# Kernel optimization log

Hardware: AMD Instinct MI355X
Metric: run time of the kernel (lower is better)

Reference implementation:

```python
import jax, jax.numpy as jnp
import numpy as np

N_NODES = 50000


def gcn_layer(x, W, b, src, dst, num_nodes):
    """PyG-style GCNConv: add self-loops, symmetric normalization, linear, scatter-add, bias."""
    # linear transform first (PyG applies lin before propagate)
    h = x @ W  # [N, out]
    # add self loops
    loop = jnp.arange(num_nodes, dtype=src.dtype)
    s = jnp.concatenate([src, loop])  # [E+N]
    d = jnp.concatenate([dst, loop])  # [E+N]
    # degree of target nodes (with self loops)
    deg = jax.ops.segment_sum(jnp.ones_like(d, dtype=h.dtype), d, num_segments=num_nodes)
    dis = jnp.where(deg > 0, jax.lax.rsqrt(deg), 0.0)  # deg^{-1/2}
    norm = dis[s] * dis[d]  # [E+N]
    msg = h[s] * norm[:, None]  # gather + scale: [E+N, out]
    out = jax.ops.segment_sum(msg, d, num_segments=num_nodes)  # scatter-add
    return out + b


def setup_inputs() -> dict:
    key = jax.random.key(0)
    ks = jax.random.split(key, 8)
    n, e = N_NODES, 800000
    in_c, hid_c, out_c = 64, 128, 64
    x = jax.random.normal(ks[0], (n, in_c), dtype=jnp.float32)
    edge_index = jax.random.randint(ks[1], (2, e), 0, n, dtype=jnp.int64)
    def glorot(k, fan_in, fan_out):
        lim = np.sqrt(6.0 / (fan_in + fan_out)).astype(np.float32)
        return jax.random.uniform(k, (fan_in, fan_out), jnp.float32, -lim, lim)
    return {
        "x": x,
        "edge_index": edge_index,
        "W1": glorot(ks[2], in_c, hid_c), "b1": jnp.zeros((hid_c,), jnp.float32),
        "W2": glorot(ks[3], hid_c, hid_c), "b2": jnp.zeros((hid_c,), jnp.float32),
        "W3": glorot(ks[4], hid_c, out_c), "b3": jnp.zeros((out_c,), jnp.float32),
    }


def reference(x, edge_index, W1, b1, W2, b2, W3, b3):
    src, dst = edge_index[0], edge_index[1]
    n = x.shape[0]
    h = gcn_layer(x, W1, b1, src, dst, n)
    h = jax.nn.relu(h)
    h = gcn_layer(h, W2, b2, src, dst, n)
    h = jax.nn.relu(h)
    return gcn_layer(h, W3, b3, src, dst, n)
```

## Files before the change

### kernel.cpp

```cpp
#include <hip/hip_runtime.h>
#include <hip/hip_fp16.h>


typedef _Float16 h8 __attribute__((ext_vector_type(8)));
typedef float f32x4 __attribute__((ext_vector_type(4)));

struct alignas(8) Half4 { __half2 lo, hi; };

__device__ inline float4 h4_to_f4(Half4 h) {
    float2 a = __half22float2(h.lo), b = __half22float2(h.hi);
    return make_float4(a.x, a.y, b.x, b.y);
}
__device__ inline Half4 f4_to_h4(float4 v) {
    Half4 h; h.lo = __floats2half2_rn(v.x, v.y); h.hi = __floats2half2_rn(v.z, v.w); return h;
}

#define MAXNB 512


__global__ __launch_bounds__(256) void bucket_count(const int* __restrict__ dst,
                                                    int* __restrict__ bcnt, int e, int nb) {
    __shared__ int h[MAXNB];
    int tid = threadIdx.x;
    for (int i = tid; i < nb; i += 256) h[i] = 0;
    __syncthreads();
    for (int i = blockIdx.x * 256 + tid; i < e; i += gridDim.x * 256)
        atomicAdd(&h[dst[i] >> 7], 1);
    __syncthreads();
    for (int i = tid; i < nb; i += 256) {
        int c = h[i];
        if (c) atomicAdd(&bcnt[i], c);
    }
}


__global__ void scan_buckets(const int* __restrict__ bcnt, int* __restrict__ bbase,
                             int* __restrict__ bcursor, int nb) {
    int lane = threadIdx.x;
    int running = 0;
    for (int base = 0; base < nb; base += 64) {
        int idx = base + lane;
        int v = (idx < nb) ? bcnt[idx] : 0;
        int x = v;
        #pragma unroll
        for (int d = 1; d < 64; d <<= 1) {
            int t = __shfl_up(x, d, 64);
            if (lane >= d) x += t;
        }
        if (idx < nb) { bbase[idx] = running + x - v; bcursor[idx] = running + x - v; }
        running += __shfl(x, 63, 64);
    }
    if (lane == 0) bbase[nb] = running;
}


#define R3_CHUNK 4096

__global__ __launch_bounds__(256) void bin_edges(const int* __restrict__ src,
                                                 const int* __restrict__ dst,
                                                 int* __restrict__ bcursor,
                                                 int2* __restrict__ binned, int e, int nb) {
    __shared__ int h[MAXNB];
    __shared__ int gp[MAXNB];
    int tid = threadIdx.x;
    for (int i = tid; i < nb; i += 256) h[i] = 0;
    __syncthreads();
    int lo = blockIdx.x * R3_CHUNK, hi = min(lo + R3_CHUNK, e);
    for (int i = lo + tid; i < hi; i += 256) atomicAdd(&h[dst[i] >> 7], 1);
    __syncthreads();
    for (int b = tid; b < nb; b += 256) {
        int c = h[b];
        if (c) gp[b] = atomicAdd(&bcursor[b], c);
        h[b] = 0;
    }
    __syncthreads();
    for (int i = lo + tid; i < hi; i += 256) {
        int d = dst[i];
        int b = d >> 7;
        int p = atomicAdd(&h[b], 1);
        binned[gp[b] + p] = make_int2(src[i], d);
    }
}


__global__ __launch_bounds__(128) void finalize_csr(const int2* __restrict__ binned,
                                                    const int* __restrict__ bbase,
                                                    int* __restrict__ offsets,
                                                    int* __restrict__ srcs,
                                                    float* __restrict__ dis,
                                                    int n, int nb) {
    int b = blockIdx.x;
    int tid = threadIdx.x;
    int nb0 = b << 7;
    int segLo = bbase[b], segHi = bbase[b + 1];

    __shared__ int cnt[128];
    __shared__ int cur[128];
    __shared__ int wtot;
    cnt[tid] = 0;
    __syncthreads();
    for (int i = segLo + tid; i < segHi; i += 128)
        atomicAdd(&cnt[binned[i].y & 127], 1);
    __syncthreads();

    int c = cnt[tid];
    int lane = tid & 63, w = tid >> 6;
    int x = c;
    #pragma unroll
    for (int d = 1; d < 64; d <<= 1) {
        int t = __shfl_up(x, d, 64);
        if (lane >= d) x += t;
    }
    if (w == 0 && lane == 63) wtot = x;
    __syncthreads();
    int excl = x - c + (w ? wtot : 0);

    int node = nb0 + tid;
    if (node < n) {
        offsets[node] = segLo + excl;
        dis[node] = rsqrtf((float)(c + 1));
    }
    if (b == nb - 1 && tid == 0) offsets[n] = segHi;
    cur[tid] = excl;
    __syncthreads();

    for (int i = segLo + tid; i < segHi; i += 128) {
        int2 v = binned[i];
        int ln = v.y & 127;
        int p = atomicAdd(&cur[ln], 1);
        srcs[segLo + p] = v.x;
    }
}


__global__ __launch_bounds__(256) void prep_x_kernel(const float* __restrict__ x,
                                                     const float* __restrict__ dis,
                                                     Half4* __restrict__ x16, int n) {
    int gid = blockIdx.x * 256 + threadIdx.x;
    int total = n * 16;
    if (gid >= total) return;
    int node = gid >> 4;
    float4 v = reinterpret_cast<const float4*>(x)[gid];
    float d = dis[node];
    x16[gid] = f4_to_h4(make_float4(v.x * d, v.y * d, v.z * d, v.w * d));
}


template<int C, bool RELU, bool BIAS, bool OUTH>
__global__ __launch_bounds__(256) void aggregate_h(const __half* __restrict__ g,
                                                   const int* __restrict__ srcs,
                                                   const int* __restrict__ offsets,
                                                   const float* __restrict__ dis,
                                                   const float* __restrict__ bias,
                                                   void* __restrict__ outv, int n) {
    int wid = threadIdx.x >> 6, lane = threadIdx.x & 63;
    int i = blockIdx.x * 4 + wid;
    if (i >= n) return;
    float di = dis[i];
    int e0 = offsets[i], e1 = offsets[i + 1];
    int e = e0;

    if constexpr (C == 128) {
        int half_ = lane >> 5, cl = lane & 31, c = cl * 4;
        const Half4* gc = reinterpret_cast<const Half4*>(g) + cl;
        float4 a0 = make_float4(0.f, 0.f, 0.f, 0.f), a1v = a0, a2 = a0, a3 = a0;

        if (half_ == 0) a0 = h4_to_f4(gc[(size_t)i * 32]);

        for (; e + 8 <= e1; e += 8) {
            int s0 = srcs[e + half_], s1 = srcs[e + 2 + half_];
            int s2 = srcs[e + 4 + half_], s3 = srcs[e + 6 + half_];
            float4 l0 = h4_to_f4(gc[(size_t)s0 * 32]);
            float4 l1 = h4_to_f4(gc[(size_t)s1 * 32]);
            float4 l2 = h4_to_f4(gc[(size_t)s2 * 32]);
            float4 l3 = h4_to_f4(gc[(size_t)s3 * 32]);
            a0.x += l0.x; a0.y += l0.y; a0.z += l0.z; a0.w += l0.w;
            a1v.x += l1.x; a1v.y += l1.y; a1v.z += l1.z; a1v.w += l1.w;
            a2.x += l2.x; a2.y += l2.y; a2.z += l2.z; a2.w += l2.w;
            a3.x += l3.x; a3.y += l3.y; a3.z += l3.z; a3.w += l3.w;
        }
        if (e + 4 <= e1) {
            int s0 = srcs[e + half_], s1 = srcs[e + 2 + half_];
            float4 l0 = h4_to_f4(gc[(size_t)s0 * 32]);
            float4 l1 = h4_to_f4(gc[(size_t)s1 * 32]);
            a0.x += l0.x; a0.y += l0.y; a0.z += l0.z; a0.w += l0.w;
            a1v.x += l1.x; a1v.y += l1.y; a1v.z += l1.z; a1v.w += l1.w;
            e += 4;
        }
        if (e + 2 <= e1) {
            int s0 = srcs[e + half_];
            float4 l0 = h4_to_f4(gc[(size_t)s0 * 32]);
            a2.x += l0.x; a2.y += l0.y; a2.z += l0.z; a2.w += l0.w;
            e += 2;
        }
        if (e < e1 && half_ == 0) {
            int s0 = srcs[e];
            float4 l0 = h4_to_f4(gc[(size_t)s0 * 32]);
            a3.x += l0.x; a3.y += l0.y; a3.z += l0.z; a3.w += l0.w;
        }

        float4 acc = make_float4((a0.x + a1v.x) + (a2.x + a3.x), (a0.y + a1v.y) + (a2.y + a3.y),
                                 (a0.z + a1v.z) + (a2.z + a3.z), (a0.w + a1v.w) + (a2.w + a3.w));
        acc.x += __shfl_xor(acc.x, 32, 64);
        acc.y += __shfl_xor(acc.y, 32, 64);
        acc.z += __shfl_xor(acc.z, 32, 64);
        acc.w += __shfl_xor(acc.w, 32, 64);

        if (half_ == 0) {
            float4 o = make_float4(di * acc.x, di * acc.y, di * acc.z, di * acc.w);
            if constexpr (BIAS) {
                float4 b = *reinterpret_cast<const float4*>(bias + c);
                o.x += b.x; o.y += b.y; o.z += b.z; o.w += b.w;
            }
            if constexpr (RELU) {
                o.x = fmaxf(o.x, 0.f); o.y = fmaxf(o.y, 0.f);
                o.z = fmaxf(o.z, 0.f); o.w = fmaxf(o.w, 0.f);
            }
            if constexpr (OUTH)
                *reinterpret_cast<Half4*>((__half*)outv + (size_t)i * C + c) = f4_to_h4(o);
            else
                *reinterpret_cast<float4*>((float*)outv + (size_t)i * C + c) = o;
        }
    } else {
        int grp = lane >> 4, cl = lane & 15, c = cl * 4;
        const Half4* gc = reinterpret_cast<const Half4*>(g) + cl;
        float4 a0 = make_float4(0.f, 0.f, 0.f, 0.f), a1v = a0;

        if (grp == 0) a0 = h4_to_f4(gc[(size_t)i * 16]);

        for (; e + 8 <= e1; e += 8) {
            int s0 = srcs[e + grp], s1 = srcs[e + 4 + grp];
            float4 l0 = h4_to_f4(gc[(size_t)s0 * 16]);
            float4 l1 = h4_to_f4(gc[(size_t)s1 * 16]);
            a0.x += l0.x; a0.y += l0.y; a0.z += l0.z; a0.w += l0.w;
            a1v.x += l1.x; a1v.y += l1.y; a1v.z += l1.z; a1v.w += l1.w;
        }
        if (e + 4 <= e1) {
            int s0 = srcs[e + grp];
            float4 l0 = h4_to_f4(gc[(size_t)s0 * 16]);
            a0.x += l0.x; a0.y += l0.y; a0.z += l0.z; a0.w += l0.w;
            e += 4;
        }
        int rem = e1 - e;
        if (grp < rem) {
            int s0 = srcs[e + grp];
            float4 l0 = h4_to_f4(gc[(size_t)s0 * 16]);
            a1v.x += l0.x; a1v.y += l0.y; a1v.z += l0.z; a1v.w += l0.w;
        }

        float4 acc = make_float4(a0.x + a1v.x, a0.y + a1v.y, a0.z + a1v.z, a0.w + a1v.w);
        #pragma unroll
        for (int d = 16; d <= 32; d <<= 1) {
            acc.x += __shfl_xor(acc.x, d, 64);
            acc.y += __shfl_xor(acc.y, d, 64);
            acc.z += __shfl_xor(acc.z, d, 64);
            acc.w += __shfl_xor(acc.w, d, 64);
        }

        if (grp == 0) {
            float4 o = make_float4(di * acc.x, di * acc.y, di * acc.z, di * acc.w);
            if constexpr (BIAS) {
                float4 b = *reinterpret_cast<const float4*>(bias + c);
                o.x += b.x; o.y += b.y; o.z += b.z; o.w += b.w;
            }
            if constexpr (RELU) {
                o.x = fmaxf(o.x, 0.f); o.y = fmaxf(o.y, 0.f);
                o.z = fmaxf(o.z, 0.f); o.w = fmaxf(o.w, 0.f);
            }
            if constexpr (OUTH)
                *reinterpret_cast<Half4*>((__half*)outv + (size_t)i * C + c) = f4_to_h4(o);
            else
                *reinterpret_cast<float4*>((float*)outv + (size_t)i * C + c) = o;
        }
    }
}


template<int CIN, int COUT>
__global__ __launch_bounds__(256) void pack_w(const float* __restrict__ W, h8* __restrict__ Wp) {
    constexpr int NKS = CIN / 32, NCT = COUT / 16;
    int idx = blockIdx.x * 256 + threadIdx.x;
    if (idx >= NKS * NCT * 64) return;
    int l = idx & 63;
    int ct = (idx >> 6) % NCT;
    int ks = (idx >> 6) / NCT;
    int col = ct * 16 + (l & 15);
    int kb = ks * 32 + ((l >> 4) << 2);
    h8 t;
    #pragma unroll
    for (int j = 0; j < 8; ++j) {
        int k = kb + (j & 3) + ((j >> 2) << 4);
        t[j] = (_Float16)W[k * COUT + col];
    }
    Wp[idx] = t;
}


template<int CIN, int COUT, int EPI>
__global__ __launch_bounds__(256) void mfma_gemm(const __half* __restrict__ A,
                                                 const h8* __restrict__ Wp,
                                                 const float* __restrict__ aux,
                                                 __half* __restrict__ out, int n) {
    constexpr int NKS = CIN / 32, NCT = COUT / 16;
    constexpr int FRAGS = NKS * NCT * 64;
    __shared__ h8 wlds[FRAGS];
    for (int idx = threadIdx.x; idx < FRAGS; idx += 256) wlds[idx] = Wp[idx];
    __syncthreads();

    int wid = threadIdx.x >> 6, lane = threadIdx.x & 63;
    int rowBase = blockIdx.x * 128 + wid * 32;
    int m = lane & 15;
    int kq = (lane >> 4) << 2;

    int row0 = min(rowBase + m, n - 1);
    int row1 = min(rowBase + 16 + m, n - 1);
    const __half* ar0 = A + (size_t)row0 * CIN;
    const __half* ar1 = A + (size_t)row1 * CIN;

    f32x4 acc[2][NCT];
    #pragma unroll
    for (int rt = 0; rt < 2; ++rt)
        #pragma unroll
        for (int ct = 0; ct < NCT; ++ct)
            acc[rt][ct] = f32x4{0.f, 0.f, 0.f, 0.f};

    #pragma unroll
    for (int ks = 0; ks < NKS; ++ks) {
        int kb = ks * 32 + kq;
        h8 a0, a1;
        *reinterpret_cast<short4*>(&a0) = *reinterpret_cast<const short4*>(ar0 + kb);
        *(reinterpret_cast<short4*>(&a0) + 1) = *reinterpret_cast<const short4*>(ar0 + kb + 16);
        *reinterpret_cast<short4*>(&a1) = *reinterpret_cast<const short4*>(ar1 + kb);
        *(reinterpret_cast<short4*>(&a1) + 1) = *reinterpret_cast<const short4*>(ar1 + kb + 16);
        #pragma unroll
        for (int ct = 0; ct < NCT; ++ct) {
            h8 b = wlds[(ks * NCT + ct) * 64 + lane];
            acc[0][ct] = __builtin_amdgcn_mfma_f32_16x16x32_f16(a0, b, acc[0][ct], 0, 0, 0);
            acc[1][ct] = __builtin_amdgcn_mfma_f32_16x16x32_f16(a1, b, acc[1][ct], 0, 0, 0);
        }
    }

    float bcol[NCT];
    if constexpr (EPI == 1) {
        #pragma unroll
        for (int ct = 0; ct < NCT; ++ct) bcol[ct] = aux[ct * 16 + m];
    }
    #pragma unroll
    for (int rt = 0; rt < 2; ++rt) {
        #pragma unroll
        for (int r = 0; r < 4; ++r) {
            int row = rowBase + rt * 16 + kq + r;
            if (row < n) {
                float d = 0.f;
                if constexpr (EPI == 0) d = aux[row];
                __half* orow = out + (size_t)row * COUT + m;
                #pragma unroll
                for (int ct = 0; ct < NCT; ++ct) {
                    float v = acc[rt][ct][r];
                    if constexpr (EPI == 0) v *= d;
                    else v = fmaxf(v + bcol[ct], 0.f);
                    orow[ct * 16] = __float2half(v);
                }
            }
        }
    }
}


extern "C" void kernel_launch(void* const* d_in, const int* in_sizes, int n_in,
                              void* d_out, int out_size, void* d_ws, size_t ws_size,
                              hipStream_t stream) {
    const float* x  = (const float*)d_in[0];
    const int*   ei = (const int*)d_in[1];
    const float* W1 = (const float*)d_in[2];
    const float* b1 = (const float*)d_in[3];
    const float* W2 = (const float*)d_in[4];
    const float* b2 = (const float*)d_in[5];
    const float* W3 = (const float*)d_in[6];
    const float* b3 = (const float*)d_in[7];

    const int n = in_sizes[0] / 64;
    const int e = in_sizes[1] / 2;
    const int* src = ei;
    const int* dst = ei + e;
    const int nb = (n + 127) >> 7;

    int*   ws_i = (int*)d_ws;
    float* ws_f = (float*)d_ws;
    size_t o = 0;
    int* bcnt    = ws_i + o; o += MAXNB;
    int* bbase   = ws_i + o; o += MAXNB + 2;
    int* bcursor = ws_i + o; o += MAXNB;
    int* offsets = ws_i + o; o += n + 8;
    int* srcs    = ws_i + o; o += e;
    float* dis   = ws_f + o; o += n;
    o = (o + 1) & ~(size_t)1;
    int2* binned = (int2*)(ws_i + o); o += (size_t)e * 2;
    o = (o + 3) & ~(size_t)3;
    h8* Wp1 = (h8*)(ws_i + o); o += 4096;
    h8* Wp2 = (h8*)(ws_i + o); o += 8192;
    h8* Wp3 = (h8*)(ws_i + o); o += 4096;
    float* R1 = ws_f + o; o += (size_t)n * 64;
    float* R2 = ws_f + o; o += (size_t)n * 64;

    Half4*  x16 = (Half4*)d_out;
    __half* g2  = (__half*)d_out;
    __half* a1h = (__half*)R1;
    __half* h1h = (__half*)R2;
    __half* h2h = (__half*)R1;
    __half* g3  = (__half*)R2;
    float*  out = (float*)d_out;

    const int B = 256;
    hipMemsetAsync(bcnt, 0, MAXNB * sizeof(int), stream);
    bucket_count<<<256, B, 0, stream>>>(dst, bcnt, e, nb);
    scan_buckets<<<1, 64, 0, stream>>>(bcnt, bbase, bcursor, nb);
    bin_edges<<<(e + R3_CHUNK - 1) / R3_CHUNK, B, 0, stream>>>(src, dst, bcursor, binned, e, nb);
    finalize_csr<<<nb, 128, 0, stream>>>(binned, bbase, offsets, srcs, dis, n, nb);
    prep_x_kernel<<<(n * 16 + B - 1) / B, B, 0, stream>>>(x, dis, x16, n);
    pack_w<64, 128><<<4, B, 0, stream>>>(W1, Wp1);
    pack_w<128, 128><<<8, B, 0, stream>>>(W2, Wp2);
    pack_w<128, 64><<<4, B, 0, stream>>>(W3, Wp3);

    dim3 agrid((n + 3) / 4);
    dim3 ggrid((n + 127) / 128);

    aggregate_h<64, false, false, true><<<agrid, 256, 0, stream>>>((const __half*)x16, srcs, offsets, dis, nullptr, a1h, n);
    mfma_gemm<64, 128, 1><<<ggrid, 256, 0, stream>>>(a1h, Wp1, b1, h1h, n);
    mfma_gemm<128, 128, 0><<<ggrid, 256, 0, stream>>>(h1h, Wp2, dis, g2, n);
    aggregate_h<128, true, true, true><<<agrid, 256, 0, stream>>>(g2, srcs, offsets, dis, b2, h2h, n);
    mfma_gemm<128, 64, 0><<<ggrid, 256, 0, stream>>>(h2h, Wp3, dis, g3, n);
    aggregate_h<64, false, true, false><<<agrid, 256, 0, stream>>>(g3, srcs, offsets, dis, b3, out, n);
}
```

Measured before the change: 178.7 us.

## Pack binned edges to 32-bit, fuse x prescale into CSR finalize, merge weight packing

When node indices fit in 16 bits, the binned edge records shrink from an int2 to a single 32-bit word holding the 16-bit source and the 7-bit local destination. This halves the write and read traffic of the binning stage. The separate x-scaling and half-conversion kernel is folded into finalize_csr, using degree values kept in shared memory. The three weight-packing launches become one kernel. Together these cut launches and memory traffic in preprocessing, but the fused x conversion runs with only 128 threads per block on the finalize grid.

```diff
diff --git a/kernel.cpp b/kernel.cpp
--- a/kernel.cpp
+++ b/kernel.cpp
@@ -56,10 +56,11 @@
 
 #define R3_CHUNK 4096
 
+template<bool PACKED>
 __global__ __launch_bounds__(256) void bin_edges(const int* __restrict__ src,
                                                  const int* __restrict__ dst,
                                                  int* __restrict__ bcursor,
-                                                 int2* __restrict__ binned, int e, int nb) {
+                                                 void* __restrict__ binned_, int e, int nb) {
     __shared__ int h[MAXNB];
     __shared__ int gp[MAXNB];
     int tid = threadIdx.x;
@@ -78,16 +79,22 @@
         int d = dst[i];
         int b = d >> 7;
         int p = atomicAdd(&h[b], 1);
-        binned[gp[b] + p] = make_int2(src[i], d);
-    }
-}
-
-
-__global__ __launch_bounds__(128) void finalize_csr(const int2* __restrict__ binned,
+        if constexpr (PACKED)
+            ((unsigned*)binned_)[gp[b] + p] = (unsigned)src[i] | ((unsigned)(d & 127) << 16);
+        else
+            ((int2*)binned_)[gp[b] + p] = make_int2(src[i], d);
+    }
+}
+
+
+template<bool PACKED>
+__global__ __launch_bounds__(128) void finalize_csr(const void* __restrict__ binned_,
                                                     const int* __restrict__ bbase,
                                                     int* __restrict__ offsets,
                                                     int* __restrict__ srcs,
                                                     float* __restrict__ dis,
+                                                    const float* __restrict__ x,
+                                                    Half4* __restrict__ x16,
                                                     int n, int nb) {
     int b = blockIdx.x;
     int tid = threadIdx.x;
@@ -96,53 +103,73 @@
 
     __shared__ int cnt[128];
     __shared__ int cur[128];
+    __shared__ float sdis[128];
     __shared__ int wtot;
     cnt[tid] = 0;
     __syncthreads();
-    for (int i = segLo + tid; i < segHi; i += 128)
-        atomicAdd(&cnt[binned[i].y & 127], 1);
+    if constexpr (PACKED) {
+        const unsigned* binned = (const unsigned*)binned_;
+        for (int i = segLo + tid; i < segHi; i += 128)
+            atomicAdd(&cnt[(binned[i] >> 16) & 127], 1);
+    } else {
+        const int2* binned = (const int2*)binned_;
+        for (int i = segLo + tid; i < segHi; i += 128)
+            atomicAdd(&cnt[binned[i].y & 127], 1);
+    }
     __syncthreads();
 
     int c = cnt[tid];
     int lane = tid & 63, w = tid >> 6;
-    int x = c;
+    int x_ = c;
     #pragma unroll
     for (int d = 1; d < 64; d <<= 1) {
-        int t = __shfl_up(x, d, 64);
-        if (lane >= d) x += t;
-    }
-    if (w == 0 && lane == 63) wtot = x;
-    __syncthreads();
-    int excl = x - c + (w ? wtot : 0);
+        int t = __shfl_up(x_, d, 64);
+        if (lane >= d) x_ += t;
+    }
+    if (w == 0 && lane == 63) wtot = x_;
+    __syncthreads();
+    int excl = x_ - c + (w ? wtot : 0);
 
     int node = nb0 + tid;
+    float dv = rsqrtf((float)(c + 1));
     if (node < n) {
         offsets[node] = segLo + excl;
-        dis[node] = rsqrtf((float)(c + 1));
+        dis[node] = dv;
     }
     if (b == nb - 1 && tid == 0) offsets[n] = segHi;
     cur[tid] = excl;
-    __syncthreads();
-
-    for (int i = segLo + tid; i < segHi; i += 128) {
-        int2 v = binned[i];
-        int ln = v.y & 127;
-        int p = atomicAdd(&cur[ln], 1);
-        srcs[segLo + p] = v.x;
-    }
-}
-
-
-__global__ __launch_bounds__(256) void prep_x_kernel(const float* __restrict__ x,
-                                                     const float* __restrict__ dis,
-                                                     Half4* __restrict__ x16, int n) {
-    int gid = blockIdx.x * 256 + threadIdx.x;
-    int total = n * 16;
-    if (gid >= total) return;
-    int node = gid >> 4;
-    float4 v = reinterpret_cast<const float4*>(x)[gid];
-    float d = dis[node];
-    x16[gid] = f4_to_h4(make_float4(v.x * d, v.y * d, v.z * d, v.w * d));
+    sdis[tid] = dv;
+    __syncthreads();
+
+    if constexpr (PACKED) {
+        const unsigned* binned = (const unsigned*)binned_;
+        for (int i = segLo + tid; i < segHi; i += 128) {
+            unsigned v = binned[i];
+            int ln = (v >> 16) & 127;
+            int p = atomicAdd(&cur[ln], 1);
+            srcs[segLo + p] = (int)(v & 0xFFFFu);
+        }
+    } else {
+        const int2* binned = (const int2*)binned_;
+        for (int i = segLo + tid; i < segHi; i += 128) {
+            int2 v = binned[i];
+            int ln = v.y & 127;
+            int p = atomicAdd(&cur[ln], 1);
+            srcs[segLo + p] = v.x;
+        }
+    }
+
+    int rows = min(128, n - nb0);
+    if (rows > 0) {
+        int limit = rows * 16;
+        const float4* xr = reinterpret_cast<const float4*>(x) + (size_t)nb0 * 16;
+        Half4* xo = x16 + (size_t)nb0 * 16;
+        for (int idx = tid; idx < limit; idx += 128) {
+            float d = sdis[idx >> 4];
+            float4 v = xr[idx];
+            xo[idx] = f4_to_h4(make_float4(v.x * d, v.y * d, v.z * d, v.w * d));
+        }
+    }
 }
 
 
@@ -277,10 +304,8 @@
 
 
 template<int CIN, int COUT>
-__global__ __launch_bounds__(256) void pack_w(const float* __restrict__ W, h8* __restrict__ Wp) {
-    constexpr int NKS = CIN / 32, NCT = COUT / 16;
-    int idx = blockIdx.x * 256 + threadIdx.x;
-    if (idx >= NKS * NCT * 64) return;
+__device__ inline void pack_frag(const float* __restrict__ W, h8* __restrict__ Wp, int idx) {
+    constexpr int NCT = COUT / 16;
     int l = idx & 63;
     int ct = (idx >> 6) % NCT;
     int ks = (idx >> 6) / NCT;
@@ -293,6 +318,17 @@
         t[j] = (_Float16)W[k * COUT + col];
     }
     Wp[idx] = t;
+}
+
+__global__ __launch_bounds__(256) void pack_all(const float* __restrict__ W1,
+                                                const float* __restrict__ W2,
+                                                const float* __restrict__ W3,
+                                                h8* __restrict__ Wp1, h8* __restrict__ Wp2,
+                                                h8* __restrict__ Wp3) {
+    int idx = blockIdx.x * 256 + threadIdx.x;
+    if (idx < 1024)      pack_frag<64, 128>(W1, Wp1, idx);
+    else if (idx < 3072) pack_frag<128, 128>(W2, Wp2, idx - 1024);
+    else if (idx < 4096) pack_frag<128, 64>(W3, Wp3, idx - 3072);
 }
 
 
@@ -384,6 +420,7 @@
     const int* src = ei;
     const int* dst = ei + e;
     const int nb = (n + 127) >> 7;
+    const bool packed = (n <= 65536);
 
     int*   ws_i = (int*)d_ws;
     float* ws_f = (float*)d_ws;
@@ -395,7 +432,7 @@
     int* srcs    = ws_i + o; o += e;
     float* dis   = ws_f + o; o += n;
     o = (o + 1) & ~(size_t)1;
-    int2* binned = (int2*)(ws_i + o); o += (size_t)e * 2;
+    void* binned = (void*)(ws_i + o); o += (size_t)e * 2;
     o = (o + 3) & ~(size_t)3;
     h8* Wp1 = (h8*)(ws_i + o); o += 4096;
     h8* Wp2 = (h8*)(ws_i + o); o += 8192;
@@ -415,12 +452,14 @@
     hipMemsetAsync(bcnt, 0, MAXNB * sizeof(int), stream);
     bucket_count<<<256, B, 0, stream>>>(dst, bcnt, e, nb);
     scan_buckets<<<1, 64, 0, stream>>>(bcnt, bbase, bcursor, nb);
-    bin_edges<<<(e + R3_CHUNK - 1) / R3_CHUNK, B, 0, stream>>>(src, dst, bcursor, binned, e, nb);
-    finalize_csr<<<nb, 128, 0, stream>>>(binned, bbase, offsets, srcs, dis, n, nb);
-    prep_x_kernel<<<(n * 16 + B - 1) / B, B, 0, stream>>>(x, dis, x16, n);
-    pack_w<64, 128><<<4, B, 0, stream>>>(W1, Wp1);
-    pack_w<128, 128><<<8, B, 0, stream>>>(W2, Wp2);
-    pack_w<128, 64><<<4, B, 0, stream>>>(W3, Wp3);
+    if (packed) {
+        bin_edges<true><<<(e + R3_CHUNK - 1) / R3_CHUNK, B, 0, stream>>>(src, dst, bcursor, binned, e, nb);
+        finalize_csr<true><<<nb, 128, 0, stream>>>(binned, bbase, offsets, srcs, dis, x, x16, n, nb);
+    } else {
+        bin_edges<false><<<(e + R3_CHUNK - 1) / R3_CHUNK, B, 0, stream>>>(src, dst, bcursor, binned, e, nb);
+        finalize_csr<false><<<nb, 128, 0, stream>>>(binned, bbase, offsets, srcs, dis, x, x16, n, nb);
+    }
+    pack_all<<<16, B, 0, stream>>>(W1, W2, W3, Wp1, Wp2, Wp3);
 
     dim3 agrid((n + 3) / 4);
     dim3 ggrid((n + 127) / 128);
```

Result: no change. 177.3 us (-0.8%).
